# Optimization experiments

Hardware: AMD Instinct MI355X
Metric: run time of the kernel (lower is better)

The kernel has to match this reference:

```python
import jax, jax.numpy as jnp
import numpy as np

IN_FEATURES = 4096
OUT_FEATURES = 768
N_BITS = 8
SCALE = float(2 ** N_BITS - 1)  # 255
REG_WEIGHT = 0.001


def setup_inputs() -> dict:
    key = jax.random.key(0)
    k1, k2, k3 = jax.random.split(key, 3)
    latent = jax.random.normal(k1, (1024, IN_FEATURES), dtype=jnp.float32)
    true_sum = jax.random.uniform(k2, (1024, OUT_FEATURES * N_BITS), dtype=jnp.float32)
    # nn.init.uniform_(weight, -0.1, 0.1)
    weight = jax.random.uniform(k3, (IN_FEATURES, OUT_FEATURES * N_BITS),
                                dtype=jnp.float32, minval=-0.1, maxval=0.1)
    return {"latent": latent, "true_sum": true_sum, "weight": weight}


def _powers():
    # [1, 2, 4, ..., 2^(n-1)] with the top (sign) bit negated -> two's complement
    p = 2.0 ** jnp.arange(N_BITS, dtype=jnp.float32)
    return p.at[-1].multiply(-1.0)


def reference(latent, true_sum, weight):
    prob_weights = jax.nn.sigmoid(weight)                      # [in, out*n_bits]
    # min(|p-0|, |p-1|) = min(p, 1-p) for p in (0,1)
    reg_loss = REG_WEIGHT * jnp.minimum(prob_weights, 1.0 - prob_weights).mean()

    powers = _powers()                                         # [n_bits]
    int_weights = jnp.einsum('iob,b->io',
                             prob_weights.reshape(IN_FEATURES, -1, N_BITS),
                             powers)                           # [in, out]
    int_sum = jnp.einsum('nob,b->no',
                         true_sum.reshape(true_sum.shape[0], -1, N_BITS),
                         powers)                               # [B, out]

    # (latent[:, :, None] * int_weights[None]).sum(-2) == latent @ int_weights
    pred = jnp.einsum('bi,io->bo', latent, int_weights)        # [B, out]

    recon_loss = jnp.mean((pred / SCALE - int_sum / SCALE) ** 2)
    return (recon_loss + reg_loss, recon_loss, reg_loss)
```

## Files before the change

### kernel.cpp

```cpp
#include <hip/hip_runtime.h>
#include <hip/hip_bf16.h>
#include <stdint.h>

#define IN_F   4096
#define OUT_F  768
#define OUTB   (OUT_F * 8)
#define BATCH  1024
#define SPLITK 4
#define KSPAN  (IN_F / SPLITK)
#define KGSPAN (KSPAN / 8)
#define NIT    (KSPAN / 64)
#define PLANE  (BATCH * OUT_F)
#define PLANE4 (PLANE / 4)
#define EPIBLK 768

typedef short short8  __attribute__((ext_vector_type(8)));
typedef float f32x4   __attribute__((ext_vector_type(4)));

#define WS_WP    12582912
#define WS_LAT   18874368
#define WS_REGP  27262976
#define WS_SQP   27269120

__device__ __forceinline__ ushort f2bf(float f) {
    uint32_t u = __builtin_bit_cast(uint32_t, f);
    u += 0x7FFFu + ((u >> 16) & 1u);
    return (ushort)(u >> 16);
}

__device__ __forceinline__ float waveReduceSum(float v) {
    #pragma unroll
    for (int off = 32; off > 0; off >>= 1) v += __shfl_down(v, off, 64);
    return v;
}

__global__ __launch_bounds__(256) void k_weights(const float* __restrict__ w,
                                                 const float* __restrict__ latent,
                                                 ushort* __restrict__ wp,
                                                 ushort* __restrict__ laT,
                                                 float* __restrict__ regpart) {
    if (blockIdx.x >= 1536) {
        int t = (blockIdx.x - 1536) * 256 + threadIdx.x;
        int m = t & 1023;
        int kg0 = (t >> 10) << 2;
        const float4* src = (const float4*)(latent + (size_t)m * IN_F + kg0 * 8);
        #pragma unroll
        for (int j = 0; j < 4; j++) {
            float4 x0 = src[2 * j];
            float4 x1 = src[2 * j + 1];
            union { ushort u[8]; uint4 v; } pk;
            pk.u[0] = f2bf(x0.x); pk.u[1] = f2bf(x0.y); pk.u[2] = f2bf(x0.z); pk.u[3] = f2bf(x0.w);
            pk.u[4] = f2bf(x1.x); pk.u[5] = f2bf(x1.y); pk.u[6] = f2bf(x1.z); pk.u[7] = f2bf(x1.w);
            *(uint4*)(laT + (((size_t)(kg0 + j) << 10) + m) * 8) = pk.v;
        }
        return;
    }

    int t  = blockIdx.x * 256 + threadIdx.x;
    int o  = t % OUT_F;
    int i8 = t / OUT_F;
    const float* src = w + (size_t)(i8 * 8) * OUTB + (size_t)o * 8;

    const float P[8] = {1.f, 2.f, 4.f, 8.f, 16.f, 32.f, 64.f, -128.f};
    float regsum = 0.f;
    union { ushort u[8]; uint4 v; } pk;

    #pragma unroll
    for (int r = 0; r < 8; r++) {
        float4 a = *(const float4*)(src + (size_t)r * OUTB);
        float4 b = *(const float4*)(src + (size_t)r * OUTB + 4);
        float x[8] = {a.x, a.y, a.z, a.w, b.x, b.y, b.z, b.w};
        float iw = 0.f;
        #pragma unroll
        for (int j = 0; j < 8; j++) {
            float p = __builtin_amdgcn_rcpf(1.f + __expf(-x[j]));
            iw += p * P[j];
            regsum += fminf(p, 1.f - p);
        }
        pk.u[r] = f2bf(iw);
    }
    *(uint4*)(wp + ((size_t)i8 * OUT_F + o) * 8) = pk.v;

    float ws = waveReduceSum(regsum);
    __shared__ float red[4];
    int lane = threadIdx.x & 63, wv = threadIdx.x >> 6;
    if (lane == 0) red[wv] = ws;
    __syncthreads();
    if (threadIdx.x == 0) regpart[blockIdx.x] = red[0] + red[1] + red[2] + red[3];
}

#define LOAD_SET(A_, B_, it) do {                                              \
    _Pragma("unroll") for (int s_ = 0; s_ < 2; s_++) {                         \
        _Pragma("unroll") for (int f_ = 0; f_ < 2; f_++) {                     \
            A_[s_][f_] = *(const short8*)(aB + (size_t)((it) * 8 + s_ * 4) * 8192 + f_ * 128); \
            B_[s_][f_] = *(const short8*)(bB + (size_t)((it) * 8 + s_ * 4) * 6144 + f_ * 128); \
        } } } while (0)

#define MFMA_SET(A_, B_) do {                                                  \
    _Pragma("unroll") for (int s_ = 0; s_ < 2; s_++)                           \
    _Pragma("unroll") for (int fm_ = 0; fm_ < 2; fm_++)                        \
    _Pragma("unroll") for (int fn_ = 0; fn_ < 2; fn_++)                        \
        acc[fm_][fn_] = __builtin_amdgcn_mfma_f32_16x16x32_bf16(               \
            A_[s_][fm_], B_[s_][fn_], acc[fm_][fn_], 0, 0, 0); } while (0)

__global__ __launch_bounds__(256, 3) void k_gemm(const ushort* __restrict__ laT,
                                                 const ushort* __restrict__ wp,
                                                 float* __restrict__ predp) {
    const int tid  = threadIdx.x;
    const int n0   = blockIdx.x * 64;
    const int m0   = blockIdx.y * 64;
    const int kgb  = blockIdx.z * KGSPAN;
    const int lane = tid & 63, w = tid >> 6;
    const int wm = w >> 1, wn = w & 1;
    const int quad = lane >> 4, l16 = lane & 15;

    f32x4 acc[2][2] = {{{0.f,0.f,0.f,0.f},{0.f,0.f,0.f,0.f}},
                       {{0.f,0.f,0.f,0.f},{0.f,0.f,0.f,0.f}}};

    const ushort* aB = laT + (((size_t)(kgb + quad) << 10) + m0 + wm * 32 + l16) * 8;
    const ushort* bB = wp  + ((size_t)(kgb + quad) * OUT_F + n0 + wn * 32 + l16) * 8;

    short8 a0[2][2], b0[2][2], a1[2][2], b1[2][2];
    LOAD_SET(a0, b0, 0);
    #pragma unroll
    for (int it = 0; it < NIT; it += 2) {
        LOAD_SET(a1, b1, it + 1);
        MFMA_SET(a0, b0);
        if (it + 2 < NIT) LOAD_SET(a0, b0, it + 2);
        MFMA_SET(a1, b1);
    }

    float* plane = predp + (size_t)blockIdx.z * PLANE;
    #pragma unroll
    for (int fm = 0; fm < 2; fm++)
    #pragma unroll
    for (int fn = 0; fn < 2; fn++)
    #pragma unroll
    for (int r = 0; r < 4; r++) {
        int m = m0 + wm * 32 + fm * 16 + quad * 4 + r;
        int n = n0 + wn * 32 + fn * 16 + l16;
        plane[(size_t)m * OUT_F + n] = acc[fm][fn][r];
    }
}

__global__ __launch_bounds__(256) void k_epi(const float* __restrict__ predp,
                                             const float* __restrict__ tsum,
                                             float* __restrict__ sqpart) {
    int g = blockIdx.x * 256 + threadIdx.x;
    int m = g / (OUT_F / 4);
    int c = g % (OUT_F / 4);
    const float4* pp = (const float4*)predp;
    float4 p0 = pp[g];
    float4 p1 = pp[g + PLANE4];
    float4 p2 = pp[g + 2 * PLANE4];
    float4 p3 = pp[g + 3 * PLANE4];
    float pv[4] = {p0.x + p1.x + p2.x + p3.x, p0.y + p1.y + p2.y + p3.y,
                   p0.z + p1.z + p2.z + p3.z, p0.w + p1.w + p2.w + p3.w};
    const float* ts = tsum + (size_t)m * OUTB + (size_t)c * 32;
    float lsum = 0.f;
    #pragma unroll
    for (int j = 0; j < 4; j++) {
        float4 t0 = *(const float4*)(ts + j * 8);
        float4 t1 = *(const float4*)(ts + j * 8 + 4);
        float isum = t0.x + 2.f * t0.y + 4.f * t0.z + 8.f * t0.w
                   + 16.f * t1.x + 32.f * t1.y + 64.f * t1.z - 128.f * t1.w;
        float d = pv[j] - isum;
        lsum += d * d;
    }
    float wsum = waveReduceSum(lsum);
    __shared__ float red[4];
    if ((threadIdx.x & 63) == 0) red[threadIdx.x >> 6] = wsum;
    __syncthreads();
    if (threadIdx.x == 0)
        sqpart[blockIdx.x] = red[0] + red[1] + red[2] + red[3];
}

__global__ __launch_bounds__(256) void k_fin(const float* __restrict__ regpart,
                                             const float* __restrict__ sqpart,
                                             float* __restrict__ out) {
    int tid = threadIdx.x;
    float r = 0.f, s = 0.f;
    #pragma unroll
    for (int j = 0; j < 6; j++) r += regpart[tid + j * 256];
    #pragma unroll
    for (int j = 0; j < 3; j++) s += sqpart[tid + j * 256];
    r = waveReduceSum(r);
    s = waveReduceSum(s);
    __shared__ float redR[4], redS[4];
    int lane = tid & 63, wv = tid >> 6;
    if (lane == 0) { redR[wv] = r; redS[wv] = s; }
    __syncthreads();
    if (tid == 0) {
        float R = redR[0] + redR[1] + redR[2] + redR[3];
        float S = redS[0] + redS[1] + redS[2] + redS[3];
        float recon = S / ((float)(BATCH * OUT_F) * 255.f * 255.f);
        float reg   = 0.001f * R / (float)((size_t)IN_F * OUTB);
        out[0] = recon + reg;
        out[1] = recon;
        out[2] = reg;
    }
}

extern "C" void kernel_launch(void* const* d_in, const int* in_sizes, int n_in,
                              void* d_out, int out_size, void* d_ws, size_t ws_size,
                              hipStream_t stream) {
    const float* latent = (const float*)d_in[0];
    const float* tsum   = (const float*)d_in[1];
    const float* weight = (const float*)d_in[2];
    float* out      = (float*)d_out;
    float* predp    = (float*)d_ws;
    ushort* wp      = (ushort*)((char*)d_ws + WS_WP);
    ushort* laT     = (ushort*)((char*)d_ws + WS_LAT);
    float* regpart  = (float*)((char*)d_ws + WS_REGP);
    float* sqpart   = (float*)((char*)d_ws + WS_SQP);

    k_weights<<<2048, 256, 0, stream>>>(weight, latent, wp, laT, regpart);
    k_gemm<<<dim3(OUT_F / 64, BATCH / 64, SPLITK), 256, 0, stream>>>(laT, wp, predp);
    k_epi<<<EPIBLK, 256, 0, stream>>>(predp, tsum, sqpart);
    k_fin<<<1, 256, 0, stream>>>(regpart, sqpart, out);
}
```

Baseline: 201.1 us.

## Drop split-K and fuse loss epilogue into GEMM

```diff
diff --git a/kernel.cpp b/kernel.cpp
--- a/kernel.cpp
+++ b/kernel.cpp
@@ -6,21 +6,16 @@
 #define OUT_F  768
 #define OUTB   (OUT_F * 8)
 #define BATCH  1024
-#define SPLITK 4
-#define KSPAN  (IN_F / SPLITK)
-#define KGSPAN (KSPAN / 8)
-#define NIT    (KSPAN / 64)
-#define PLANE  (BATCH * OUT_F)
-#define PLANE4 (PLANE / 4)
-#define EPIBLK 768
+#define NKG    (IN_F / 8)
+#define NIT    (IN_F / 64)
+#define NTILE  192
 
 typedef short short8  __attribute__((ext_vector_type(8)));
 typedef float f32x4   __attribute__((ext_vector_type(4)));
 
-#define WS_WP    12582912
-#define WS_LAT   18874368
-#define WS_REGP  27262976
-#define WS_SQP   27269120
+#define WS_LAT   6291456
+#define WS_REGP  14680064
+#define WS_SQP   14686208
 
 __device__ __forceinline__ ushort f2bf(float f) {
     uint32_t u = __builtin_bit_cast(uint32_t, f);
@@ -103,13 +98,13 @@
         acc[fm_][fn_] = __builtin_amdgcn_mfma_f32_16x16x32_bf16(               \
             A_[s_][fm_], B_[s_][fn_], acc[fm_][fn_], 0, 0, 0); } while (0)
 
-__global__ __launch_bounds__(256, 3) void k_gemm(const ushort* __restrict__ laT,
-                                                 const ushort* __restrict__ wp,
-                                                 float* __restrict__ predp) {
+__global__ __launch_bounds__(256) void k_gemm(const ushort* __restrict__ laT,
+                                              const ushort* __restrict__ wp,
+                                              const float* __restrict__ tsum,
+                                              float* __restrict__ sqpart) {
     const int tid  = threadIdx.x;
     const int n0   = blockIdx.x * 64;
     const int m0   = blockIdx.y * 64;
-    const int kgb  = blockIdx.z * KGSPAN;
     const int lane = tid & 63, w = tid >> 6;
     const int wm = w >> 1, wn = w & 1;
     const int quad = lane >> 4, l16 = lane & 15;
@@ -117,12 +112,11 @@
     f32x4 acc[2][2] = {{{0.f,0.f,0.f,0.f},{0.f,0.f,0.f,0.f}},
                        {{0.f,0.f,0.f,0.f},{0.f,0.f,0.f,0.f}}};
 
-    const ushort* aB = laT + (((size_t)(kgb + quad) << 10) + m0 + wm * 32 + l16) * 8;
-    const ushort* bB = wp  + ((size_t)(kgb + quad) * OUT_F + n0 + wn * 32 + l16) * 8;
+    const ushort* aB = laT + (((size_t)quad << 10) + m0 + wm * 32 + l16) * 8;
+    const ushort* bB = wp  + ((size_t)quad * OUT_F + n0 + wn * 32 + l16) * 8;
 
     short8 a0[2][2], b0[2][2], a1[2][2], b1[2][2];
     LOAD_SET(a0, b0, 0);
-    #pragma unroll
     for (int it = 0; it < NIT; it += 2) {
         LOAD_SET(a1, b1, it + 1);
         MFMA_SET(a0, b0);
@@ -130,7 +124,7 @@
         MFMA_SET(a1, b1);
     }
 
-    float* plane = predp + (size_t)blockIdx.z * PLANE;
+    float lsum = 0.f;
     #pragma unroll
     for (int fm = 0; fm < 2; fm++)
     #pragma unroll
@@ -139,51 +133,30 @@
     for (int r = 0; r < 4; r++) {
         int m = m0 + wm * 32 + fm * 16 + quad * 4 + r;
         int n = n0 + wn * 32 + fn * 16 + l16;
-        plane[(size_t)m * OUT_F + n] = acc[fm][fn][r];
-    }
-}
-
-__global__ __launch_bounds__(256) void k_epi(const float* __restrict__ predp,
-                                             const float* __restrict__ tsum,
-                                             float* __restrict__ sqpart) {
-    int g = blockIdx.x * 256 + threadIdx.x;
-    int m = g / (OUT_F / 4);
-    int c = g % (OUT_F / 4);
-    const float4* pp = (const float4*)predp;
-    float4 p0 = pp[g];
-    float4 p1 = pp[g + PLANE4];
-    float4 p2 = pp[g + 2 * PLANE4];
-    float4 p3 = pp[g + 3 * PLANE4];
-    float pv[4] = {p0.x + p1.x + p2.x + p3.x, p0.y + p1.y + p2.y + p3.y,
-                   p0.z + p1.z + p2.z + p3.z, p0.w + p1.w + p2.w + p3.w};
-    const float* ts = tsum + (size_t)m * OUTB + (size_t)c * 32;
-    float lsum = 0.f;
-    #pragma unroll
-    for (int j = 0; j < 4; j++) {
-        float4 t0 = *(const float4*)(ts + j * 8);
-        float4 t1 = *(const float4*)(ts + j * 8 + 4);
+        const float* ts = tsum + (size_t)m * OUTB + (size_t)n * 8;
+        float4 t0 = *(const float4*)ts;
+        float4 t1 = *(const float4*)(ts + 4);
         float isum = t0.x + 2.f * t0.y + 4.f * t0.z + 8.f * t0.w
                    + 16.f * t1.x + 32.f * t1.y + 64.f * t1.z - 128.f * t1.w;
-        float d = pv[j] - isum;
+        float d = acc[fm][fn][r] - isum;
         lsum += d * d;
     }
     float wsum = waveReduceSum(lsum);
     __shared__ float red[4];
-    if ((threadIdx.x & 63) == 0) red[threadIdx.x >> 6] = wsum;
+    if ((tid & 63) == 0) red[tid >> 6] = wsum;
     __syncthreads();
-    if (threadIdx.x == 0)
-        sqpart[blockIdx.x] = red[0] + red[1] + red[2] + red[3];
+    if (tid == 0)
+        sqpart[blockIdx.y * 12 + blockIdx.x] = red[0] + red[1] + red[2] + red[3];
 }
 
 __global__ __launch_bounds__(256) void k_fin(const float* __restrict__ regpart,
                                              const float* __restrict__ sqpart,
                                              float* __restrict__ out) {
     int tid = threadIdx.x;
-    float r = 0.f, s = 0.f;
+    float r = 0.f;
     #pragma unroll
     for (int j = 0; j < 6; j++) r += regpart[tid + j * 256];
-    #pragma unroll
-    for (int j = 0; j < 3; j++) s += sqpart[tid + j * 256];
+    float s = (tid < NTILE) ? sqpart[tid] : 0.f;
     r = waveReduceSum(r);
     s = waveReduceSum(s);
     __shared__ float redR[4], redS[4];
@@ -208,14 +181,12 @@
     const float* tsum   = (const float*)d_in[1];
     const float* weight = (const float*)d_in[2];
     float* out      = (float*)d_out;
-    float* predp    = (float*)d_ws;
-    ushort* wp      = (ushort*)((char*)d_ws + WS_WP);
+    ushort* wp      = (ushort*)d_ws;
     ushort* laT     = (ushort*)((char*)d_ws + WS_LAT);
     float* regpart  = (float*)((char*)d_ws + WS_REGP);
     float* sqpart   = (float*)((char*)d_ws + WS_SQP);
 
     k_weights<<<2048, 256, 0, stream>>>(weight, latent, wp, laT, regpart);
-    k_gemm<<<dim3(OUT_F / 64, BATCH / 64, SPLITK), 256, 0, stream>>>(laT, wp, predp);
-    k_epi<<<EPIBLK, 256, 0, stream>>>(predp, tsum, sqpart);
+    k_gemm<<<dim3(OUT_F / 64, BATCH / 64), 256, 0, stream>>>(laT, wp, tsum, sqpart);
     k_fin<<<1, 256, 0, stream>>>(regpart, sqpart, out);
 }
```

After: 203.8 us. About the same (+1.3%).
